# Kernel tuning notes

Measured on AMD Instinct MI355X. Metric: run time of the kernel, lower is better.

## Reference

```python
import jax, jax.numpy as jnp
import numpy as np
import math

B, L, H, E = 16, 1024, 8, 64   # L = nsensor = N (forced by einsum 'bhls,bhlg')
WIN = 1024                      # win_size, last dim of x
G = 64                          # n_group
D_SEL = 1                       # d_sel default


def setup_inputs() -> dict:
    key = jax.random.key(0)
    ks = jax.random.split(key, 7)
    return {
        "queries": jax.random.normal(ks[0], (B, L, H, E), dtype=jnp.float32),
        "keys": jax.random.normal(ks[1], (B, L, H, E), dtype=jnp.float32),
        "values": jax.random.normal(ks[2], (B, L, H, E), dtype=jnp.float32),
        "x": jax.random.normal(ks[3], (B, L, WIN), dtype=jnp.float32),
        "mlp_w": jax.random.normal(ks[4], (H * D_SEL, WIN), dtype=jnp.float32) * 0.02,
        "mlp_b": jax.random.normal(ks[5], (H * D_SEL,), dtype=jnp.float32) * 0.02,
        "sel_W": jax.random.normal(ks[6], (H, G, D_SEL), dtype=jnp.float32),
        "attn_mask": 0,
    }


def _select_attention(x, mlp_w, mlp_b, sel_W, n_heads, d_sel):
    b, n, lwin = x.shape
    xf = x.reshape(b * n, lwin)
    newx = jnp.tanh(xf @ mlp_w.T + mlp_b)                 # [(B*N), H*d_sel]
    # Faithful raw reshape (torch.reshape, no permute): mixes n and h axes.
    newx = newx.reshape(b, n_heads, n, d_sel)             # [B, H, N, d_sel]
    sel = jnp.einsum('bhnd,hgd->bhng', newx, sel_W)       # [B, H, N, G]
    return jax.nn.relu(sel)


def reference(queries, keys, values, x, mlp_w, mlp_b, sel_W, attn_mask):
    b, l, h, e = queries.shape
    scale = 1.0 / math.sqrt(e)
    scores = jnp.einsum('blhe,bshe->bhls', queries, keys)      # [B, H, L, S]
    sel = _select_attention(x, mlp_w, mlp_b, sel_W, h, D_SEL)  # [B, H, L, G]
    scores = jnp.einsum('bhls,bhlg->bhsg', scores, sel)        # [B, H, S, G]
    series = jax.nn.softmax(scale * scores, axis=-1)           # softmax over groups
    # values labeled 'blhs': l=S (value len), s=D (feature). Output V: [B, D, H, G]
    V = jnp.einsum('blhs,bhlg->bshg', values, series)
    return V
```

## Files before the change

### kernel.cpp

```cpp
#include <hip/hip_runtime.h>
#include <math.h>

#define NB 16
#define NL 1024
#define NH 8
#define NE 64
#define NWIN 1024
#define NG 64

#define SCH 256
#define VROW 264

typedef __attribute__((ext_vector_type(8))) short short8;
typedef __attribute__((ext_vector_type(4))) float floatx4;

__device__ __forceinline__ float wave_sum(float v) {
    #pragma unroll
    for (int off = 32; off > 0; off >>= 1) v += __shfl_xor(v, off, 64);
    return v;
}

__device__ __forceinline__ short f2bf(float x) {
    unsigned u = __float_as_uint(x);
    u += 0x7fffu + ((u >> 16) & 1u);
    return (short)(u >> 16);
}

__global__ __launch_bounds__(256) void k_tanh_mlp(
    const float* __restrict__ x, const float* __restrict__ mlp_w,
    const float* __restrict__ mlp_b, float* __restrict__ t_out)
{
    __shared__ float4 w_lds[8][NWIN / 4];
    int tid = threadIdx.x;
    const float4* w4 = (const float4*)mlp_w;
    float4* wl = (float4*)w_lds;
    #pragma unroll
    for (int i = 0; i < 8; ++i)
        wl[tid + 256 * i] = w4[tid + 256 * i];
    __syncthreads();

    int wave = tid >> 6, lane = tid & 63;
    int r = blockIdx.x * 4 + wave;
    const float4* xr = (const float4*)(x + (size_t)r * NWIN);
    float acc[8] = {0.f,0.f,0.f,0.f,0.f,0.f,0.f,0.f};
    #pragma unroll
    for (int it = 0; it < 4; ++it) {
        float4 xv = xr[it * 64 + lane];
        #pragma unroll
        for (int c = 0; c < 8; ++c) {
            float4 wv = w_lds[c][it * 64 + lane];
            acc[c] += xv.x * wv.x + xv.y * wv.y + xv.z * wv.z + xv.w * wv.w;
        }
    }
    #pragma unroll
    for (int c = 0; c < 8; ++c) acc[c] = wave_sum(acc[c]);
    if (lane == 0) {
        int b = r >> 10, rr = r & 1023;
        int h = rr >> 7, l8 = rr & 127;
        float* dst = t_out + ((b * NH + h) * NL) + l8 * 8;
        #pragma unroll
        for (int c = 0; c < 8; ++c)
            dst[c] = tanhf(acc[c] + mlp_b[c]);
    }
}

__global__ __launch_bounds__(256) void k_qpn(
    const float* __restrict__ q, const float* __restrict__ t,
    float* __restrict__ qp, float* __restrict__ qn)
{
    int blk = blockIdx.x;
    int lc = blk & 7;
    int bh = blk >> 3;
    int b = bh >> 3, h = bh & 7;
    int wave = threadIdx.x >> 6, lane = threadIdx.x & 63;
    int lo = lane >> 4, e4 = lane & 15;
    const float* tb = t + bh * NL;
    float4 accp = make_float4(0.f,0.f,0.f,0.f);
    float4 accn = make_float4(0.f,0.f,0.f,0.f);
    int lbase = lc * 128 + wave * 32;
    #pragma unroll
    for (int i = 0; i < 8; ++i) {
        int l = lbase + i * 4 + lo;
        float tv = tb[l];
        float4 qv = *(const float4*)(q + (((size_t)(b * NL + l)) * NH + h) * NE + e4 * 4);
        float tp = fmaxf(tv, 0.f), tn = fminf(tv, 0.f);
        accp.x = fmaf(tp, qv.x, accp.x); accp.y = fmaf(tp, qv.y, accp.y);
        accp.z = fmaf(tp, qv.z, accp.z); accp.w = fmaf(tp, qv.w, accp.w);
        accn.x = fmaf(tn, qv.x, accn.x); accn.y = fmaf(tn, qv.y, accn.y);
        accn.z = fmaf(tn, qv.z, accn.z); accn.w = fmaf(tn, qv.w, accn.w);
    }
    #pragma unroll
    for (int off = 16; off <= 32; off <<= 1) {
        accp.x += __shfl_xor(accp.x, off, 64); accp.y += __shfl_xor(accp.y, off, 64);
        accp.z += __shfl_xor(accp.z, off, 64); accp.w += __shfl_xor(accp.w, off, 64);
        accn.x += __shfl_xor(accn.x, off, 64); accn.y += __shfl_xor(accn.y, off, 64);
        accn.z += __shfl_xor(accn.z, off, 64); accn.w += __shfl_xor(accn.w, off, 64);
    }
    __shared__ float redp[4][64], redn[4][64];
    if (lo == 0) {
        *(float4*)&redp[wave][e4 * 4] = accp;
        *(float4*)&redn[wave][e4 * 4] = accn;
    }
    __syncthreads();
    if (threadIdx.x < 64) {
        int e = threadIdx.x;
        atomicAdd(&qp[bh * NE + e], redp[0][e] + redp[1][e] + redp[2][e] + redp[3][e]);
    } else if (threadIdx.x < 128) {
        int e = threadIdx.x - 64;
        atomicAdd(&qn[bh * NE + e], redn[0][e] + redn[1][e] + redn[2][e] + redn[3][e]);
    }
}

__global__ __launch_bounds__(256) void k_attn_out(
    const float* __restrict__ keys, const float* __restrict__ values,
    const float* __restrict__ sel_W,
    const float* __restrict__ qp, const float* __restrict__ qn,
    float* __restrict__ out)
{
    __shared__ short vb[NE][VROW];
    __shared__ short sb[NG][VROW];
    __shared__ float ap_l[SCH], an_l[SCH];
    __shared__ float2 wpn[NG];

    int blk = blockIdx.x;
    int chunk = blk & 3;
    int bh = blk >> 2;
    int b = bh >> 3, h = bh & 7;
    int tid = threadIdx.x;
    int w = tid >> 6, lane = tid & 63;
    const float scale = 0.125f;

    if (tid < NG) {
        float W = sel_W[h * NG + tid];
        wpn[tid] = make_float2(fmaxf(W, 0.f) * scale, fminf(W, 0.f) * scale);
    }

    int c = lane & 15, sq = lane >> 4;
    const float4 qp4 = *(const float4*)(qp + bh * NE + c * 4);
    const float4 qn4 = *(const float4*)(qn + bh * NE + c * 4);

    #pragma unroll 4
    for (int p_ = 0; p_ < 16; ++p_) {
        int sl = w * 64 + p_ * 4 + sq;
        int s = chunk * SCH + sl;
        float4 kv = *(const float4*)(keys + (((size_t)(b * NL + s)) * NH + h) * NE + c * 4);
        float pp = kv.x * qp4.x + kv.y * qp4.y + kv.z * qp4.z + kv.w * qp4.w;
        float pn = kv.x * qn4.x + kv.y * qn4.y + kv.z * qn4.z + kv.w * qn4.w;
        #pragma unroll
        for (int m_ = 1; m_ <= 8; m_ <<= 1) {
            pp += __shfl_xor(pp, m_, 64);
            pn += __shfl_xor(pn, m_, 64);
        }
        if (c == 0) { ap_l[sl] = pp; an_l[sl] = pn; }
    }

    #pragma unroll 4
    for (int i = 0; i < 64; ++i) {
        int sl = w * 64 + i;
        int s = chunk * SCH + sl;
        float v = values[(((size_t)(b * NL + s)) * NH + h) * NE + lane];
        vb[lane][sl] = f2bf(v);
    }
    __syncthreads();

    {
        int sl = w * 64 + lane;
        float ap = ap_l[sl], an = an_l[sl];
        float m = -INFINITY;
        #pragma unroll 8
        for (int g = 0; g < NG; ++g) {
            float2 wv = wpn[g];
            float lg = wv.x * ap + wv.y * an;
            m = fmaxf(m, lg);
        }
        float d = 0.f;
        #pragma unroll 8
        for (int g = 0; g < NG; ++g) {
            float2 wv = wpn[g];
            float lg = wv.x * ap + wv.y * an;
            d += __expf(lg - m);
        }
        float inv = 1.0f / d;
        #pragma unroll 8
        for (int g = 0; g < NG; ++g) {
            float2 wv = wpn[g];
            float lg = wv.x * ap + wv.y * an;
            sb[g][sl] = f2bf(__expf(lg - m) * inv);
        }
    }
    __syncthreads();

    floatx4 acc[4] = {{0.f,0.f,0.f,0.f},{0.f,0.f,0.f,0.f},
                      {0.f,0.f,0.f,0.f},{0.f,0.f,0.f,0.f}};
    int kq = lane >> 4;
    #pragma unroll
    for (int ks = 0; ks < SCH / 32; ++ks) {
        short8 av = *(const short8*)&vb[16 * w + c][ks * 32 + kq * 8];
        #pragma unroll
        for (int n = 0; n < 4; ++n) {
            short8 bv = *(const short8*)&sb[16 * n + c][ks * 32 + kq * 8];
            acc[n] = __builtin_amdgcn_mfma_f32_16x16x32_bf16(av, bv, acc[n], 0, 0, 0);
        }
    }

    #pragma unroll
    for (int n = 0; n < 4; ++n) {
        #pragma unroll
        for (int r = 0; r < 4; ++r) {
            int e = 16 * w + kq * 4 + r;
            int g = 16 * n + c;
            atomicAdd(&out[((size_t)(b * NE + e) * NH + h) * NG + g], acc[n][r]);
        }
    }
}

extern "C" void kernel_launch(void* const* d_in, const int* in_sizes, int n_in,
                              void* d_out, int out_size, void* d_ws, size_t ws_size,
                              hipStream_t stream) {
    (void)in_sizes; (void)n_in; (void)ws_size;
    const float* queries = (const float*)d_in[0];
    const float* keys    = (const float*)d_in[1];
    const float* values  = (const float*)d_in[2];
    const float* x       = (const float*)d_in[3];
    const float* mlp_w   = (const float*)d_in[4];
    const float* mlp_b   = (const float*)d_in[5];
    const float* sel_W   = (const float*)d_in[6];
    float* out = (float*)d_out;

    float* t_ws = (float*)d_ws;
    float* qp_ws = t_ws + NB * NH * NL;
    float* qn_ws = qp_ws + NB * NH * NE;

    hipMemsetAsync(out, 0, (size_t)out_size * sizeof(float), stream);
    hipMemsetAsync(qp_ws, 0, (size_t)2 * NB * NH * NE * sizeof(float), stream);

    k_tanh_mlp<<<dim3(NB * NL / 4), dim3(256), 0, stream>>>(x, mlp_w, mlp_b, t_ws);
    k_qpn<<<dim3(NB * NH * 8), dim3(256), 0, stream>>>(queries, t_ws, qp_ws, qn_ws);
    k_attn_out<<<dim3(NB * NH * 4), dim3(256), 0, stream>>>(keys, values, sel_W,
                                                            qp_ws, qn_ws, out);
}
```

Before: 208.8 us.

## Fuse tanh-MLP into q-projection kernel and halve attention chunk size

Merges the tanh MLP kernel and the q-positive/negative reduction into one kernel. The tanh results stay in LDS instead of making a round trip through a global workspace, which also removes one launch. The attention kernel now uses 128-row chunks across twice as many blocks. It loads values straight from global into MFMA registers rather than staging them in LDS, and splits the softmax over groups across two half-blocks to reduce LDS use and raise occupancy. The trade-offs are strided direct loads of values, more atomic adds to the output, and fewer blocks in the fused first kernel.

```diff
diff --git a/kernel.cpp b/kernel.cpp
--- a/kernel.cpp
+++ b/kernel.cpp
@@ -8,30 +8,36 @@
 #define NWIN 1024
 #define NG 64
 
-#define SCH 256
-#define VROW 264
+#define SCH 128
+#define SROW 136
 
 typedef __attribute__((ext_vector_type(8))) short short8;
 typedef __attribute__((ext_vector_type(4))) float floatx4;
-
-__device__ __forceinline__ float wave_sum(float v) {
-    #pragma unroll
-    for (int off = 32; off > 0; off >>= 1) v += __shfl_xor(v, off, 64);
-    return v;
-}
 
 __device__ __forceinline__ short f2bf(float x) {
     unsigned u = __float_as_uint(x);
     u += 0x7fffu + ((u >> 16) & 1u);
     return (short)(u >> 16);
 }
-
-__global__ __launch_bounds__(256) void k_tanh_mlp(
+__device__ __forceinline__ float dot4(float4 a, float4 b) {
+    return fmaf(a.x, b.x, fmaf(a.y, b.y, fmaf(a.z, b.z, a.w * b.w)));
+}
+
+__global__ __launch_bounds__(256) void k_sel_q(
     const float* __restrict__ x, const float* __restrict__ mlp_w,
-    const float* __restrict__ mlp_b, float* __restrict__ t_out)
+    const float* __restrict__ mlp_b, const float* __restrict__ q,
+    float* __restrict__ qp, float* __restrict__ qn)
 {
     __shared__ float4 w_lds[8][NWIN / 4];
+    __shared__ float t_lds[256];
+    __shared__ float redp[4][64], redn[4][64];
+
     int tid = threadIdx.x;
+    int blk = blockIdx.x;
+    int qq = blk & 3, bh = blk >> 2;
+    int b = bh >> 3, h = bh & 7;
+    int w = tid >> 6, lane = tid & 63;
+
     const float4* w4 = (const float4*)mlp_w;
     float4* wl = (float4*)w_lds;
     #pragma unroll
@@ -39,49 +45,56 @@
         wl[tid + 256 * i] = w4[tid + 256 * i];
     __syncthreads();
 
-    int wave = tid >> 6, lane = tid & 63;
-    int r = blockIdx.x * 4 + wave;
-    const float4* xr = (const float4*)(x + (size_t)r * NWIN);
-    float acc[8] = {0.f,0.f,0.f,0.f,0.f,0.f,0.f,0.f};
-    #pragma unroll
-    for (int it = 0; it < 4; ++it) {
-        float4 xv = xr[it * 64 + lane];
-        #pragma unroll
-        for (int c = 0; c < 8; ++c) {
-            float4 wv = w_lds[c][it * 64 + lane];
-            acc[c] += xv.x * wv.x + xv.y * wv.y + xv.z * wv.z + xv.w * wv.w;
-        }
-    }
-    #pragma unroll
-    for (int c = 0; c < 8; ++c) acc[c] = wave_sum(acc[c]);
-    if (lane == 0) {
-        int b = r >> 10, rr = r & 1023;
-        int h = rr >> 7, l8 = rr & 127;
-        float* dst = t_out + ((b * NH + h) * NL) + l8 * 8;
-        #pragma unroll
-        for (int c = 0; c < 8; ++c)
-            dst[c] = tanhf(acc[c] + mlp_b[c]);
-    }
-}
-
-__global__ __launch_bounds__(256) void k_qpn(
-    const float* __restrict__ q, const float* __restrict__ t,
-    float* __restrict__ qp, float* __restrict__ qn)
-{
-    int blk = blockIdx.x;
-    int lc = blk & 7;
-    int bh = blk >> 3;
-    int b = bh >> 3, h = bh & 7;
-    int wave = threadIdx.x >> 6, lane = threadIdx.x & 63;
+    float4 keep03 = make_float4(0,0,0,0), keep47 = make_float4(0,0,0,0);
+    int r0 = b * 1024 + h * 128 + qq * 32 + w * 8;
+    for (int j = 0; j < 8; ++j) {
+        const float4* xr = (const float4*)(x + (size_t)(r0 + j) * NWIN);
+        float4 a03 = make_float4(0,0,0,0), a47 = make_float4(0,0,0,0);
+        #pragma unroll
+        for (int it = 0; it < 4; ++it) {
+            float4 xv = xr[it * 64 + lane];
+            a03.x += dot4(xv, w_lds[0][it * 64 + lane]);
+            a03.y += dot4(xv, w_lds[1][it * 64 + lane]);
+            a03.z += dot4(xv, w_lds[2][it * 64 + lane]);
+            a03.w += dot4(xv, w_lds[3][it * 64 + lane]);
+            a47.x += dot4(xv, w_lds[4][it * 64 + lane]);
+            a47.y += dot4(xv, w_lds[5][it * 64 + lane]);
+            a47.z += dot4(xv, w_lds[6][it * 64 + lane]);
+            a47.w += dot4(xv, w_lds[7][it * 64 + lane]);
+        }
+        #pragma unroll
+        for (int off = 1; off < 64; off <<= 1) {
+            a03.x += __shfl_xor(a03.x, off, 64);
+            a03.y += __shfl_xor(a03.y, off, 64);
+            a03.z += __shfl_xor(a03.z, off, 64);
+            a03.w += __shfl_xor(a03.w, off, 64);
+            a47.x += __shfl_xor(a47.x, off, 64);
+            a47.y += __shfl_xor(a47.y, off, 64);
+            a47.z += __shfl_xor(a47.z, off, 64);
+            a47.w += __shfl_xor(a47.w, off, 64);
+        }
+        if (lane == j) { keep03 = a03; keep47 = a47; }
+    }
+    if (lane < 8) {
+        float4 b03 = *(const float4*)mlp_b;
+        float4 b47 = *(const float4*)(mlp_b + 4);
+        float4 t03, t47;
+        t03.x = tanhf(keep03.x + b03.x); t03.y = tanhf(keep03.y + b03.y);
+        t03.z = tanhf(keep03.z + b03.z); t03.w = tanhf(keep03.w + b03.w);
+        t47.x = tanhf(keep47.x + b47.x); t47.y = tanhf(keep47.y + b47.y);
+        t47.z = tanhf(keep47.z + b47.z); t47.w = tanhf(keep47.w + b47.w);
+        *(float4*)&t_lds[w * 64 + lane * 8]     = t03;
+        *(float4*)&t_lds[w * 64 + lane * 8 + 4] = t47;
+    }
+    __syncthreads();
+
     int lo = lane >> 4, e4 = lane & 15;
-    const float* tb = t + bh * NL;
-    float4 accp = make_float4(0.f,0.f,0.f,0.f);
-    float4 accn = make_float4(0.f,0.f,0.f,0.f);
-    int lbase = lc * 128 + wave * 32;
-    #pragma unroll
-    for (int i = 0; i < 8; ++i) {
-        int l = lbase + i * 4 + lo;
-        float tv = tb[l];
+    float4 accp = make_float4(0,0,0,0), accn = make_float4(0,0,0,0);
+    #pragma unroll 4
+    for (int i = 0; i < 16; ++i) {
+        int l_loc = w * 64 + i * 4 + lo;
+        float tv = t_lds[l_loc];
+        int l = qq * 256 + l_loc;
         float4 qv = *(const float4*)(q + (((size_t)(b * NL + l)) * NH + h) * NE + e4 * 4);
         float tp = fmaxf(tv, 0.f), tn = fminf(tv, 0.f);
         accp.x = fmaf(tp, qv.x, accp.x); accp.y = fmaf(tp, qv.y, accp.y);
@@ -96,38 +109,35 @@
         accn.x += __shfl_xor(accn.x, off, 64); accn.y += __shfl_xor(accn.y, off, 64);
         accn.z += __shfl_xor(accn.z, off, 64); accn.w += __shfl_xor(accn.w, off, 64);
     }
-    __shared__ float redp[4][64], redn[4][64];
     if (lo == 0) {
-        *(float4*)&redp[wave][e4 * 4] = accp;
-        *(float4*)&redn[wave][e4 * 4] = accn;
-    }
-    __syncthreads();
-    if (threadIdx.x < 64) {
-        int e = threadIdx.x;
-        atomicAdd(&qp[bh * NE + e], redp[0][e] + redp[1][e] + redp[2][e] + redp[3][e]);
-    } else if (threadIdx.x < 128) {
-        int e = threadIdx.x - 64;
+        *(float4*)&redp[w][e4 * 4] = accp;
+        *(float4*)&redn[w][e4 * 4] = accn;
+    }
+    __syncthreads();
+    if (tid < 64) {
+        atomicAdd(&qp[bh * NE + tid], redp[0][tid] + redp[1][tid] + redp[2][tid] + redp[3][tid]);
+    } else if (tid < 128) {
+        int e = tid - 64;
         atomicAdd(&qn[bh * NE + e], redn[0][e] + redn[1][e] + redn[2][e] + redn[3][e]);
     }
 }
 
-__global__ __launch_bounds__(256) void k_attn_out(
+__global__ __launch_bounds__(256, 4) void k_attn_out(
     const float* __restrict__ keys, const float* __restrict__ values,
     const float* __restrict__ sel_W,
     const float* __restrict__ qp, const float* __restrict__ qn,
     float* __restrict__ out)
 {
-    __shared__ short vb[NE][VROW];
-    __shared__ short sb[NG][VROW];
+    __shared__ short sb[NG][SROW];
     __shared__ float ap_l[SCH], an_l[SCH];
     __shared__ float2 wpn[NG];
-
-    int blk = blockIdx.x;
-    int chunk = blk & 3;
-    int bh = blk >> 2;
+    __shared__ float mx2[2][SCH], dn2[2][SCH];
+
+    int tid = threadIdx.x, blk = blockIdx.x;
+    int chunk = blk & 7, bh = blk >> 3;
     int b = bh >> 3, h = bh & 7;
-    int tid = threadIdx.x;
     int w = tid >> 6, lane = tid & 63;
+    int c = lane & 15, sq = lane >> 4;
     const float scale = 0.125f;
 
     if (tid < NG) {
@@ -135,17 +145,16 @@
         wpn[tid] = make_float2(fmaxf(W, 0.f) * scale, fminf(W, 0.f) * scale);
     }
 
-    int c = lane & 15, sq = lane >> 4;
     const float4 qp4 = *(const float4*)(qp + bh * NE + c * 4);
     const float4 qn4 = *(const float4*)(qn + bh * NE + c * 4);
-
-    #pragma unroll 4
-    for (int p_ = 0; p_ < 16; ++p_) {
-        int sl = w * 64 + p_ * 4 + sq;
-        int s = chunk * SCH + sl;
-        float4 kv = *(const float4*)(keys + (((size_t)(b * NL + s)) * NH + h) * NE + c * 4);
-        float pp = kv.x * qp4.x + kv.y * qp4.y + kv.z * qp4.z + kv.w * qp4.w;
-        float pn = kv.x * qn4.x + kv.y * qn4.y + kv.z * qn4.z + kv.w * qn4.w;
+    int s0 = chunk * SCH;
+
+    #pragma unroll
+    for (int p = 0; p < 8; ++p) {
+        int sl = w * 32 + p * 4 + sq;
+        float4 kv = *(const float4*)(keys + (((size_t)(b * NL + s0 + sl)) * NH + h) * NE + c * 4);
+        float pp = dot4(kv, qp4);
+        float pn = dot4(kv, qn4);
         #pragma unroll
         for (int m_ = 1; m_ <= 8; m_ <<= 1) {
             pp += __shfl_xor(pp, m_, 64);
@@ -153,52 +162,52 @@
         }
         if (c == 0) { ap_l[sl] = pp; an_l[sl] = pn; }
     }
-
-    #pragma unroll 4
-    for (int i = 0; i < 64; ++i) {
-        int sl = w * 64 + i;
-        int s = chunk * SCH + sl;
-        float v = values[(((size_t)(b * NL + s)) * NH + h) * NE + lane];
-        vb[lane][sl] = f2bf(v);
-    }
     __syncthreads();
 
     {
-        int sl = w * 64 + lane;
-        float ap = ap_l[sl], an = an_l[sl];
-        float m = -INFINITY;
+        int s_ = tid & 127, gh = tid >> 7, g0 = gh * 32;
+        float ap = ap_l[s_], an = an_l[s_];
+        float m = -1e30f;
         #pragma unroll 8
-        for (int g = 0; g < NG; ++g) {
-            float2 wv = wpn[g];
-            float lg = wv.x * ap + wv.y * an;
-            m = fmaxf(m, lg);
-        }
+        for (int g = 0; g < 32; ++g) {
+            float2 wv = wpn[g0 + g];
+            m = fmaxf(m, fmaf(wv.x, ap, wv.y * an));
+        }
+        mx2[gh][s_] = m;
+        __syncthreads();
+        m = fmaxf(mx2[0][s_], mx2[1][s_]);
         float d = 0.f;
         #pragma unroll 8
-        for (int g = 0; g < NG; ++g) {
-            float2 wv = wpn[g];
-            float lg = wv.x * ap + wv.y * an;
-            d += __expf(lg - m);
-        }
-        float inv = 1.0f / d;
+        for (int g = 0; g < 32; ++g) {
+            float2 wv = wpn[g0 + g];
+            d += __expf(fmaf(wv.x, ap, wv.y * an) - m);
+        }
+        dn2[gh][s_] = d;
+        __syncthreads();
+        float inv = 1.0f / (dn2[0][s_] + dn2[1][s_]);
         #pragma unroll 8
-        for (int g = 0; g < NG; ++g) {
-            float2 wv = wpn[g];
-            float lg = wv.x * ap + wv.y * an;
-            sb[g][sl] = f2bf(__expf(lg - m) * inv);
+        for (int g = 0; g < 32; ++g) {
+            float2 wv = wpn[g0 + g];
+            sb[g0 + g][s_] = f2bf(__expf(fmaf(wv.x, ap, wv.y * an) - m) * inv);
         }
     }
     __syncthreads();
 
     floatx4 acc[4] = {{0.f,0.f,0.f,0.f},{0.f,0.f,0.f,0.f},
                       {0.f,0.f,0.f,0.f},{0.f,0.f,0.f,0.f}};
-    int kq = lane >> 4;
-    #pragma unroll
-    for (int ks = 0; ks < SCH / 32; ++ks) {
-        short8 av = *(const short8*)&vb[16 * w + c][ks * 32 + kq * 8];
+    const float* vbase = values + (((size_t)(b * NL + s0)) * NH + h) * NE + 16 * w + c;
+    #pragma unroll
+    for (int ks = 0; ks < 4; ++ks) {
+        float a[8];
+        #pragma unroll
+        for (int j = 0; j < 8; ++j)
+            a[j] = vbase[(size_t)(ks * 32 + sq * 8 + j) * (NH * NE)];
+        short8 av;
+        #pragma unroll
+        for (int j = 0; j < 8; ++j) av[j] = f2bf(a[j]);
         #pragma unroll
         for (int n = 0; n < 4; ++n) {
-            short8 bv = *(const short8*)&sb[16 * n + c][ks * 32 + kq * 8];
+            short8 bv = *(const short8*)&sb[16 * n + c][ks * 32 + sq * 8];
             acc[n] = __builtin_amdgcn_mfma_f32_16x16x32_bf16(av, bv, acc[n], 0, 0, 0);
         }
     }
@@ -207,7 +216,7 @@
     for (int n = 0; n < 4; ++n) {
         #pragma unroll
         for (int r = 0; r < 4; ++r) {
-            int e = 16 * w + kq * 4 + r;
+            int e = 16 * w + sq * 4 + r;
             int g = 16 * n + c;
             atomicAdd(&out[((size_t)(b * NE + e) * NH + h) * NG + g], acc[n][r]);
         }
@@ -227,15 +236,14 @@
     const float* sel_W   = (const float*)d_in[6];
     float* out = (float*)d_out;
 
-    float* t_ws = (float*)d_ws;
-    float* qp_ws = t_ws + NB * NH * NL;
+    float* qp_ws = (float*)d_ws;
     float* qn_ws = qp_ws + NB * NH * NE;
 
     hipMemsetAsync(out, 0, (size_t)out_size * sizeof(float), stream);
     hipMemsetAsync(qp_ws, 0, (size_t)2 * NB * NH * NE * sizeof(float), stream);
 
-    k_tanh_mlp<<<dim3(NB * NL / 4), dim3(256), 0, stream>>>(x, mlp_w, mlp_b, t_ws);
-    k_qpn<<<dim3(NB * NH * 8), dim3(256), 0, stream>>>(queries, t_ws, qp_ws, qn_ws);
-    k_attn_out<<<dim3(NB * NH * 4), dim3(256), 0, stream>>>(keys, values, sel_W,
+    k_sel_q<<<dim3(NB * NH * 4), dim3(256), 0, stream>>>(x, mlp_w, mlp_b,
+                                                          queries, qp_ws, qn_ws);
+    k_attn_out<<<dim3(NB * NH * 8), dim3(256), 0, stream>>>(keys, values, sel_W,
                                                             qp_ws, qn_ws, out);
 }
```

Result: faster. 199.2 us (-4.6%).
